# Kernel tuning notes

Hardware: AMD Instinct MI355X
Metric: run time of the kernel (lower is better)

Reference implementation:

```python
import jax, jax.numpy as jnp
import numpy as np

N_IN, N_LAT, LEN_T, N_SHIFT = 128, 21, 51, 50
N_HID, BATCH = 4, 2048


def identity_init(n_rows, n_cols):
    A = np.zeros((n_rows, n_cols), np.float32)
    if n_rows >= n_cols:
        k = n_rows - n_cols + 1
        for c in range(n_cols):
            A[c:c + k, c] = 1.0 / k
    else:
        k = n_cols - n_rows + 1
        for r in range(n_rows):
            A[r, r:r + k] = 1.0 / k
    return jnp.asarray(A)


def setup_inputs() -> dict:
    key = jax.random.key(0)
    ks = jax.random.split(key, 8)
    s = 0.05
    return {
        'inputs': jax.random.normal(ks[0], (BATCH, LEN_T, N_IN), dtype=jnp.float32),
        'enc_W': jax.random.normal(ks[1], (N_HID, N_IN, N_IN), dtype=jnp.float32) * s,
        'enc_b': jnp.zeros((N_HID, N_IN), jnp.float32),
        'enc_Wout': jax.random.normal(ks[2], (N_IN, N_IN), dtype=jnp.float32) * s,
        'enc_bout': jnp.zeros((N_IN,), jnp.float32),
        'dec_W': jax.random.normal(ks[3], (N_HID, N_IN, N_IN), dtype=jnp.float32) * s,
        'dec_b': jnp.zeros((N_HID, N_IN), jnp.float32),
        'dec_Wout': jax.random.normal(ks[4], (N_IN, N_IN), dtype=jnp.float32) * s,
        'dec_bout': jnp.zeros((N_IN,), jnp.float32),
        'W_enc_inner': identity_init(N_IN, N_LAT),
        'L': jnp.eye(N_LAT, dtype=jnp.float32),
        'W_dec_inner': identity_init(N_LAT, N_IN),
    }


def res_block(x, Ws, bs, Wout, bout):
    # DenseResBlock: ReLU hidden dense stack + linear output + identity skip
    h = x
    for i in range(Ws.shape[0]):
        h = jax.nn.relu(h @ Ws[i] + bs[i])
    return h @ Wout + bout + x


def reference(inputs, enc_W, enc_b, enc_Wout, enc_bout,
              dec_W, dec_b, dec_Wout, dec_bout,
              W_enc_inner, L, W_dec_inner):
    B = inputs.shape[0]
    len_pred = LEN_T - N_SHIFT  # = 1

    # ---- autoencoder branch (all timesteps flattened into rows) ----
    auto_in = inputs.reshape(-1, N_IN)                       # [B*T, n_in]
    part_enc = res_block(auto_in, enc_W, enc_b, enc_Wout, enc_bout)
    full_enc = part_enc @ W_enc_inner                        # [B*T, n_lat]
    part_dec = full_enc @ W_dec_inner                        # [B*T, n_in]
    autoencoder_output = res_block(part_dec, dec_W, dec_b, dec_Wout, dec_bout)
    autoencoder_output = autoencoder_output.reshape(B, LEN_T, N_IN)
    outer_auto_output = res_block(part_enc, dec_W, dec_b, dec_Wout, dec_bout)
    outer_auto_output = outer_auto_output.reshape(B, LEN_T, N_IN)

    # ---- prediction branch: recurrent application of Koopman operator L ----
    pred_in = inputs[:, :len_pred, :].reshape(-1, N_IN)      # [B*len_pred, n_in]
    cur = res_block(pred_in, enc_W, enc_b, enc_Wout, enc_bout) @ W_enc_inner

    def step(cur_enc, _):
        adv = cur_enc @ L                                    # [B*len_pred, n_lat]
        dec = res_block(adv @ W_dec_inner, dec_W, dec_b, dec_Wout, dec_bout)
        return adv, dec

    _, preds = jax.lax.scan(step, cur, None, length=N_SHIFT)  # [S, B*lp, n_in]
    preds = preds.reshape(N_SHIFT, B, len_pred, N_IN)
    predictions = preds.transpose(1, 0, 2, 3).reshape(B, N_SHIFT * len_pred, N_IN)

    return autoencoder_output, outer_auto_output, predictions
```

## Files before the change

### kernel.cpp

```cpp
#include <hip/hip_runtime.h>
#include <stdint.h>


typedef _Float16 h8 __attribute__((ext_vector_type(8)));
typedef _Float16 h4 __attribute__((ext_vector_type(4)));
typedef float    f4 __attribute__((ext_vector_type(4)));

#define ROWS_AUTO 104448
#define NT64      1632

#define WT_ENCW      0
#define WT_ENCWOUT   (4*16384)
#define WT_DECW      (5*16384)
#define WT_DECWOUT   (9*16384)
#define WT_COMB      (10*16384)

#define MFULL_OFF_B 0x60000
#define ACH_OFF_B   0x200000
#define PE_OFF_B    0x220000
#define PD_OFF_B    0x1C00000

#define H0 0
#define H1 16384
#define H2 32768
#define LDSE 51712
#define HP 0
#define P0 16384
#define P1 32768
#define P2 49152
#define LDSP 68096

#define hsw(rl, c) ((rl)*256 + ((((c)) ^ ((rl) & 7)) << 4))

#define PIN(B) asm volatile("" : "+v"(B[0]), "+v"(B[1]), "+v"(B[2]), "+v"(B[3]), \
                                 "+v"(B[4]), "+v"(B[5]), "+v"(B[6]), "+v"(B[7]))

__device__ __forceinline__ f4 mfma16(h8 a, h8 b, f4 c) {
  return __builtin_amdgcn_mfma_f32_16x16x32_f16(a, b, c, 0, 0, 0);
}
__device__ __forceinline__ h8 cvt8(f4 a, f4 b) {
  h8 r;
  r[0]=(_Float16)a[0]; r[1]=(_Float16)a[1]; r[2]=(_Float16)a[2]; r[3]=(_Float16)a[3];
  r[4]=(_Float16)b[0]; r[5]=(_Float16)b[1]; r[6]=(_Float16)b[2]; r[7]=(_Float16)b[3];
  return r;
}
__device__ __forceinline__ void loadW(h8 B[8], const _Float16* gW, int nbase, int r15, int hi) {
#pragma unroll
  for (int nt = 0; nt < 2; ++nt)
#pragma unroll
    for (int ks = 0; ks < 4; ++ks)
      B[nt*4+ks] = *(const h8*)(gW + (size_t)(nbase + nt*16 + r15)*128 + ks*32 + hi*8);
}

__device__ __forceinline__ void mmF4s(const char* sm, int hb, const h8 B[8],
                                      f4 acc[4][2], int r15, int hi) {
#pragma unroll
  for (int rt = 0; rt < 4; ++rt) { acc[rt][0] = (f4){0,0,0,0}; acc[rt][1] = (f4){0,0,0,0}; }
#pragma unroll
  for (int ks = 0; ks < 4; ++ks) {
    int c = ks*4 + hi;
    h8 a[4];
#pragma unroll
    for (int rt = 0; rt < 4; ++rt) a[rt] = *(const h8*)(sm + hb + hsw(rt*16 + r15, c));
#pragma unroll
    for (int rt = 0; rt < 4; ++rt) {
      acc[rt][0] = mfma16(B[ks],   a[rt], acc[rt][0]);
      acc[rt][1] = mfma16(B[4+ks], a[rt], acc[rt][1]);
    }
  }
}

__device__ __forceinline__ void hw4s(char* sm, int hb, int wbase, const f4 acc[4][2],
                                     const float* bl, int bo, int r15, int hi) {
  f4 bb0 = *(const f4*)(bl + bo + wbase + hi*4);
  f4 bb1 = *(const f4*)(bl + bo + wbase + 16 + hi*4);
  int bo2 = (hi & 1) * 8;
#pragma unroll
  for (int nt = 0; nt < 2; ++nt) {
    int c = ((wbase + nt*16) >> 3) + (hi >> 1);
    f4 bb = nt ? bb1 : bb0;
#pragma unroll
    for (int rt = 0; rt < 4; ++rt) {
      int row = rt*16 + r15;
      h4 p;
#pragma unroll
      for (int d = 0; d < 4; ++d) p[d] = (_Float16)fmaxf(acc[rt][nt][d] + bb[d], 0.f);
      *(h4*)(sm + hb + row*256 + ((c ^ (row & 7)) << 4) + bo2) = p;
    }
  }
}
__device__ __forceinline__ void hw4r(char* sm, int hb, int wbase, const f4 acc[4][2],
                                     int r15, int hi) {
  int bo2 = (hi & 1) * 8;
#pragma unroll
  for (int nt = 0; nt < 2; ++nt) {
    int c = ((wbase + nt*16) >> 3) + (hi >> 1);
#pragma unroll
    for (int rt = 0; rt < 4; ++rt) {
      int row = rt*16 + r15;
      h4 p;
#pragma unroll
      for (int d = 0; d < 4; ++d) p[d] = (_Float16)acc[rt][nt][d];
      *(h4*)(sm + hb + row*256 + ((c ^ (row & 7)) << 4) + bo2) = p;
    }
  }
}


__global__ __launch_bounds__(512) void k_prep(
    const float* __restrict__ encW, const float* __restrict__ encWout,
    const float* __restrict__ decW, const float* __restrict__ decWout,
    const float* __restrict__ L,
    _Float16* __restrict__ wt, float* __restrict__ ach) {
  __shared__ float chA[441], chB[441];
  int m = blockIdx.y, tid = threadIdx.x;
  if (m == 10) {
    if (blockIdx.x != 0) return;
    if (tid < 441) chA[tid] = L[tid];
    __syncthreads();
    for (int s = 0; s < 50; ++s) {
      if (tid < 441) ach[s*441 + tid] = chA[tid];
      if (s == 49) break;
      if (tid < 441) {
        int i = tid / 21, j = tid % 21; float a = 0.f;
        for (int k = 0; k < 21; ++k) a += chA[i*21 + k] * L[k*21 + j];
        chB[tid] = a;
      }
      __syncthreads();
      if (tid < 441) chA[tid] = chB[tid];
      __syncthreads();
    }
    return;
  }
  int idx = blockIdx.x*512 + tid;
  if (idx >= 16384) return;
  const float* src; _Float16* dst;
  if (m < 4)       { src = encW + m*16384;     dst = wt + WT_ENCW + m*16384; }
  else if (m == 4) { src = encWout;            dst = wt + WT_ENCWOUT; }
  else if (m < 9)  { src = decW + (m-5)*16384; dst = wt + WT_DECW + (m-5)*16384; }
  else             { src = decWout;            dst = wt + WT_DECWOUT; }
  int n = idx >> 7, k = idx & 127;
  dst[idx] = (_Float16)src[k*128 + n];
}

__global__ __launch_bounds__(512) void k_aux(
    const float* __restrict__ ach, const float* __restrict__ wencI,
    const float* __restrict__ wdecI,
    _Float16* __restrict__ mfull, _Float16* __restrict__ wt) {
  __shared__ float T1[2688];
  __shared__ float sa[441];
  int s = blockIdx.x, t = threadIdx.x;
  if (s < 50) {
    if (t < 441) sa[t] = ach[s*441 + t];
    __syncthreads();
    for (int idx = t; idx < 2688; idx += 512) {
      int k = idx / 21, j = idx % 21;
      float a = 0.f;
      for (int u = 0; u < 21; ++u) a += wencI[k*21 + u] * sa[u*21 + j];
      T1[idx] = a;
    }
  } else {
    for (int idx = t; idx < 2688; idx += 512) T1[idx] = wencI[idx];
  }
  __syncthreads();
  _Float16* dst = (s < 50) ? (mfull + (size_t)s*16384) : (wt + WT_COMB);
  for (int idx = t; idx < 16384; idx += 512) {
    int n = idx >> 7, k = idx & 127;
    float a = 0.f;
    for (int j = 0; j < 21; ++j) a += T1[k*21 + j] * wdecI[j*128 + n];
    dst[idx] = (_Float16)a;
  }
}


__global__ __launch_bounds__(256, 2) void k_enc(
    const float* __restrict__ x, const _Float16* __restrict__ wt,
    const float* __restrict__ enc_b, const float* __restrict__ enc_bout,
    _Float16* __restrict__ pe_ws, _Float16* __restrict__ pd_ws) {
  __shared__ char sm[LDSE];
  float* bl = (float*)(sm + 49152);
  int tid = threadIdx.x, lane = tid & 63;
  int r15 = lane & 15, hi = lane >> 4;
  int wbase = (tid >> 6) * 32;
  h8 B0[8], B1[8], B2[8], B3[8], B4[8], B5[8];
  loadW(B0, wt + WT_ENCW,           wbase, r15, hi);
  loadW(B1, wt + WT_ENCW + 16384,   wbase, r15, hi);
  loadW(B2, wt + WT_ENCW + 2*16384, wbase, r15, hi);
  loadW(B3, wt + WT_ENCW + 3*16384, wbase, r15, hi);
  loadW(B4, wt + WT_ENCWOUT,        wbase, r15, hi);
  loadW(B5, wt + WT_COMB,           wbase, r15, hi);
  PIN(B0); PIN(B1); PIN(B2); PIN(B3); PIN(B4); PIN(B5);
  bl[tid] = enc_b[tid]; bl[256 + tid] = enc_b[256 + tid];
  if (tid < 128) bl[512 + tid] = enc_bout[tid];
  f4 acc[4][2];

  for (int t = blockIdx.x; t < NT64; t += gridDim.x) {
    size_t rb = (size_t)t * 64;
#pragma unroll
    for (int i = 0; i < 4; ++i) {
      int idx = i*256 + tid, rl = idx >> 4, c = idx & 15;
      const float* s = x + (rb + rl)*128 + c*8;
      f4 v0 = *(const f4*)s, v1 = *(const f4*)(s + 4);
      *(h8*)(sm + H0 + hsw(rl, c)) = cvt8(v0, v1);
    }
    __syncthreads();
    mmF4s(sm, H0, B0, acc, r15, hi); hw4s(sm, H1, wbase, acc, bl, 0,   r15, hi); __syncthreads();
    mmF4s(sm, H1, B1, acc, r15, hi); hw4s(sm, H2, wbase, acc, bl, 128, r15, hi); __syncthreads();
    mmF4s(sm, H2, B2, acc, r15, hi); hw4s(sm, H1, wbase, acc, bl, 256, r15, hi); __syncthreads();
    mmF4s(sm, H1, B3, acc, r15, hi); hw4s(sm, H2, wbase, acc, bl, 384, r15, hi); __syncthreads();
    mmF4s(sm, H2, B4, acc, r15, hi);
    {
      f4 bb0 = *(const f4*)(bl + 512 + wbase + hi*4);
      f4 bb1 = *(const f4*)(bl + 512 + wbase + 16 + hi*4);
      int bo2 = (hi & 1) * 8;
#pragma unroll
      for (int nt = 0; nt < 2; ++nt) {
        int c = ((wbase + nt*16) >> 3) + (hi >> 1);
        f4 bb = nt ? bb1 : bb0;
#pragma unroll
        for (int rt = 0; rt < 4; ++rt) {
          int row = rt*16 + r15;
          int soff = row*256 + ((c ^ (row & 7)) << 4) + bo2;
          h4 sk = *(const h4*)(sm + H0 + soff);
          h4 p;
#pragma unroll
          for (int d = 0; d < 4; ++d) p[d] = (_Float16)(acc[rt][nt][d] + bb[d] + (float)sk[d]);
          *(h4*)(sm + H1 + soff) = p;
        }
      }
    }
    __syncthreads();
    {
      char* g = (char*)(pe_ws) + (size_t)t*16384;
#pragma unroll
      for (int i = 0; i < 4; ++i) { int off = (i*256 + tid)*16;
        *(f4*)(g + off) = *(const f4*)(sm + H1 + off); }
    }
    mmF4s(sm, H1, B5, acc, r15, hi);
    hw4r(sm, H2, wbase, acc, r15, hi);
    __syncthreads();
    {
      char* g = (char*)(pd_ws) + (size_t)t*16384;
#pragma unroll
      for (int i = 0; i < 4; ++i) { int off = (i*256 + tid)*16;
        *(f4*)(g + off) = *(const f4*)(sm + H2 + off); }
    }
  }
}


__global__ __launch_bounds__(256, 2) void k_dec(
    const _Float16* __restrict__ wt, const _Float16* __restrict__ pe_ws,
    const _Float16* __restrict__ pd_ws,
    const float* __restrict__ dec_b, const float* __restrict__ dec_bout,
    float* __restrict__ out1, float* __restrict__ out2) {
  __shared__ char sm[LDSE];
  float* bl = (float*)(sm + 49152);
  int tid = threadIdx.x, lane = tid & 63;
  int r15 = lane & 15, hi = lane >> 4;
  int wbase = (tid >> 6) * 32;
  h8 B0[8], B1[8], B2[8], B3[8], B4[8];
  loadW(B0, wt + WT_DECW,           wbase, r15, hi);
  loadW(B1, wt + WT_DECW + 16384,   wbase, r15, hi);
  loadW(B2, wt + WT_DECW + 2*16384, wbase, r15, hi);
  loadW(B3, wt + WT_DECW + 3*16384, wbase, r15, hi);
  loadW(B4, wt + WT_DECWOUT,        wbase, r15, hi);
  PIN(B0); PIN(B1); PIN(B2); PIN(B3); PIN(B4);
  bl[tid] = dec_b[tid]; bl[256 + tid] = dec_b[256 + tid];
  if (tid < 128) bl[512 + tid] = dec_bout[tid];
  f4 acc[4][2];

  for (int u = blockIdx.x; u < 2*NT64; u += gridDim.x) {
    int t = (u >= NT64) ? u - NT64 : u;
    const char* src = (const char*)((u >= NT64) ? pd_ws : pe_ws) + (size_t)t*16384;
    float* dst = ((u >= NT64) ? out1 : out2) + (size_t)t*64*128;
#pragma unroll
    for (int i = 0; i < 4; ++i) {
      int off = (i*256 + tid)*16;
      *(f4*)(sm + H0 + off) = *(const f4*)(src + off);
    }
    __syncthreads();
    mmF4s(sm, H0, B0, acc, r15, hi); hw4s(sm, H1, wbase, acc, bl, 0,   r15, hi); __syncthreads();
    mmF4s(sm, H1, B1, acc, r15, hi); hw4s(sm, H2, wbase, acc, bl, 128, r15, hi); __syncthreads();
    mmF4s(sm, H2, B2, acc, r15, hi); hw4s(sm, H1, wbase, acc, bl, 256, r15, hi); __syncthreads();
    mmF4s(sm, H1, B3, acc, r15, hi); hw4s(sm, H2, wbase, acc, bl, 384, r15, hi); __syncthreads();
    mmF4s(sm, H2, B4, acc, r15, hi);
    __syncthreads();
    {
      f4 bb0 = *(const f4*)(bl + 512 + wbase + hi*4);
      f4 bb1 = *(const f4*)(bl + 512 + wbase + 16 + hi*4);
      int bo2 = (hi & 1) * 8;
#pragma unroll
      for (int nt = 0; nt < 2; ++nt) {
        int c = ((wbase + nt*16) >> 3) + (hi >> 1);
        int q = (wbase >> 2) + nt*4 + hi;
        f4 bb = nt ? bb1 : bb0;
#pragma unroll
        for (int rt = 0; rt < 4; ++rt) {
          int row = rt*16 + r15;
          h4 sk = *(const h4*)(sm + H0 + row*256 + ((c ^ (row & 7)) << 4) + bo2);
          f4 v;
#pragma unroll
          for (int d = 0; d < 4; ++d) v[d] = acc[rt][nt][d] + bb[d] + (float)sk[d];
          *(f4*)(sm + H1 + row*512 + ((q ^ ((row & 7) << 2)) << 4)) = v;
        }
      }
    }
    __syncthreads();
    {
#pragma unroll
      for (int i = 0; i < 8; ++i) {
        int idx = i*256 + tid, row = idx >> 5, q = idx & 31;
        f4 v = *(const f4*)(sm + H1 + row*512 + ((q ^ ((row & 7) << 2)) << 4));
        *(f4*)(dst + (size_t)row*128 + q*4) = v;
      }
    }
  }
}


__global__ __launch_bounds__(256, 2) void k_pred(
    const _Float16* __restrict__ pe_ws, const _Float16* __restrict__ wt,
    const _Float16* __restrict__ mfull,
    const float* __restrict__ dec_b, const float* __restrict__ dec_bout,
    float* __restrict__ out3) {
  __shared__ char sm[LDSP];
  float* bl = (float*)(sm + 65536);
  int tid = threadIdx.x, lane = tid & 63;
  int r15 = lane & 15, hi = lane >> 4;
  int wbase = (tid >> 6) * 32;
  h8 B0[8], B1[8], B2[8], B3[8], B4[8];
  loadW(B0, wt + WT_DECW,           wbase, r15, hi);
  loadW(B1, wt + WT_DECW + 16384,   wbase, r15, hi);
  loadW(B2, wt + WT_DECW + 2*16384, wbase, r15, hi);
  loadW(B3, wt + WT_DECW + 3*16384, wbase, r15, hi);
  loadW(B4, wt + WT_DECWOUT,        wbase, r15, hi);
  PIN(B0); PIN(B1); PIN(B2); PIN(B3); PIN(B4);
  bl[tid] = dec_b[tid]; bl[256 + tid] = dec_b[256 + tid];
  if (tid < 128) bl[512 + tid] = dec_bout[tid];
  f4 acc[4][2];

  int rtile = blockIdx.x / 10, chunk = blockIdx.x % 10;
#pragma unroll
  for (int i = 0; i < 4; ++i) {
    int idx = i*256 + tid, rl = idx >> 4, c = idx & 15;
    int rg = rtile*64 + rl;
    int r  = rg * 51;
    const char* sp = (const char*)pe_ws + (size_t)(r >> 6)*16384
                   + (r & 63)*256 + ((c ^ ((r & 63) & 7)) << 4);
    *(f4*)(sm + HP + hsw(rl, c)) = *(const f4*)sp;
  }
  __syncthreads();

  for (int s = chunk*5; s < chunk*5 + 5; ++s) {
    h8 Bm[8];
    loadW(Bm, mfull + (size_t)s*16384, wbase, r15, hi);
    mmF4s(sm, HP, Bm, acc, r15, hi);
    hw4r(sm, P0, wbase, acc, r15, hi);
    __syncthreads();
    mmF4s(sm, P0, B0, acc, r15, hi); hw4s(sm, P1, wbase, acc, bl, 0,   r15, hi); __syncthreads();
    mmF4s(sm, P1, B1, acc, r15, hi); hw4s(sm, P2, wbase, acc, bl, 128, r15, hi); __syncthreads();
    mmF4s(sm, P2, B2, acc, r15, hi); hw4s(sm, P1, wbase, acc, bl, 256, r15, hi); __syncthreads();
    mmF4s(sm, P1, B3, acc, r15, hi); hw4s(sm, P2, wbase, acc, bl, 384, r15, hi); __syncthreads();
    mmF4s(sm, P2, B4, acc, r15, hi);
    __syncthreads();
    {
      f4 bb0 = *(const f4*)(bl + 512 + wbase + hi*4);
      f4 bb1 = *(const f4*)(bl + 512 + wbase + 16 + hi*4);
      int bo2 = (hi & 1) * 8;
#pragma unroll
      for (int nt = 0; nt < 2; ++nt) {
        int c = ((wbase + nt*16) >> 3) + (hi >> 1);
        int q = (wbase >> 2) + nt*4 + hi;
        f4 bb = nt ? bb1 : bb0;
#pragma unroll
        for (int rt = 0; rt < 4; ++rt) {
          int row = rt*16 + r15;
          h4 sk = *(const h4*)(sm + P0 + row*256 + ((c ^ (row & 7)) << 4) + bo2);
          f4 v;
#pragma unroll
          for (int d = 0; d < 4; ++d) v[d] = acc[rt][nt][d] + bb[d] + (float)sk[d];
          *(f4*)(sm + P1 + row*512 + ((q ^ ((row & 7) << 2)) << 4)) = v;
        }
      }
    }
    __syncthreads();
    {
#pragma unroll
      for (int i = 0; i < 8; ++i) {
        int idx = i*256 + tid, row = idx >> 5, q = idx & 31;
        size_t b = (size_t)(rtile*64 + row);
        f4 v = *(const f4*)(sm + P1 + row*512 + ((q ^ ((row & 7) << 2)) << 4));
        *(f4*)(out3 + (b*50 + s)*128 + q*4) = v;
      }
    }
    __syncthreads();
  }
}


extern "C" void kernel_launch(void* const* d_in, const int* in_sizes, int n_in,
                              void* d_out, int out_size, void* d_ws, size_t ws_size,
                              hipStream_t stream) {
  const float* x        = (const float*)d_in[0];
  const float* encW     = (const float*)d_in[1];
  const float* enc_b    = (const float*)d_in[2];
  const float* encWout  = (const float*)d_in[3];
  const float* enc_bout = (const float*)d_in[4];
  const float* decW     = (const float*)d_in[5];
  const float* dec_b    = (const float*)d_in[6];
  const float* decWout  = (const float*)d_in[7];
  const float* dec_bout = (const float*)d_in[8];
  const float* wencI    = (const float*)d_in[9];
  const float* L        = (const float*)d_in[10];
  const float* wdecI    = (const float*)d_in[11];

  char* ws = (char*)d_ws;
  _Float16* wt    = (_Float16*)ws;
  _Float16* mfull = (_Float16*)(ws + MFULL_OFF_B);
  float*    ach   = (float*)(ws + ACH_OFF_B);
  _Float16* pe_ws = (_Float16*)(ws + PE_OFF_B);
  _Float16* pd_ws = (_Float16*)(ws + PD_OFF_B);

  float* out1 = (float*)d_out;
  float* out2 = out1 + (size_t)ROWS_AUTO*128;
  float* out3 = out2 + (size_t)ROWS_AUTO*128;

  hipLaunchKernelGGL(k_prep, dim3(32, 11), dim3(512), 0, stream,
                     encW, encWout, decW, decWout, L, wt, ach);
  hipLaunchKernelGGL(k_aux, dim3(51), dim3(512), 0, stream,
                     ach, wencI, wdecI, mfull, wt);
  hipLaunchKernelGGL(k_enc, dim3(512), dim3(256), 0, stream,
                     x, wt, enc_b, enc_bout, pe_ws, pd_ws);
  hipLaunchKernelGGL(k_pred, dim3(320), dim3(256), 0, stream,
                     pe_ws, wt, mfull, dec_b, dec_bout, out3);
  hipLaunchKernelGGL(k_dec, dim3(512), dim3(256), 0, stream,
                     wt, pe_ws, pd_ws, dec_b, dec_bout, out1, out2);
}
```

Baseline: 232.9 us.

## Fuse decoder and prediction kernels, recompute part_dec in-block instead of via workspace

```diff
diff --git a/kernel.cpp b/kernel.cpp
--- a/kernel.cpp
+++ b/kernel.cpp
@@ -8,6 +8,7 @@
 
 #define ROWS_AUTO 104448
 #define NT64      1632
+#define NUNITS    1952
 
 #define WT_ENCW      0
 #define WT_ENCWOUT   (4*16384)
@@ -18,17 +19,14 @@
 #define MFULL_OFF_B 0x60000
 #define ACH_OFF_B   0x200000
 #define PE_OFF_B    0x220000
-#define PD_OFF_B    0x1C00000
+#define PET0_OFF_B  0x1C00000
 
 #define H0 0
 #define H1 16384
 #define H2 32768
+#define H3 49152
 #define LDSE 51712
-#define HP 0
-#define P0 16384
-#define P1 32768
-#define P2 49152
-#define LDSP 68096
+#define LDSD 68096
 
 #define hsw(rl, c) ((rl)*256 + ((((c)) ^ ((rl) & 7)) << 4))
 
@@ -105,6 +103,43 @@
     }
   }
 }
+
+__device__ __forceinline__ void epi_store(char* sm, int hskip, int htr, int wbase,
+                                          const f4 acc[4][2], const float* bl,
+                                          float* dst, int rstride,
+                                          int tid, int r15, int hi) {
+  f4 bb0 = *(const f4*)(bl + 512 + wbase + hi*4);
+  f4 bb1 = *(const f4*)(bl + 512 + wbase + 16 + hi*4);
+  int bo2 = (hi & 1) * 8;
+#pragma unroll
+  for (int nt = 0; nt < 2; ++nt) {
+    int c = ((wbase + nt*16) >> 3) + (hi >> 1);
+    int q = (wbase >> 2) + nt*4 + hi;
+    f4 bb = nt ? bb1 : bb0;
+#pragma unroll
+    for (int rt = 0; rt < 4; ++rt) {
+      int row = rt*16 + r15;
+      h4 sk = *(const h4*)(sm + hskip + row*256 + ((c ^ (row & 7)) << 4) + bo2);
+      f4 v;
+#pragma unroll
+      for (int d = 0; d < 4; ++d) v[d] = acc[rt][nt][d] + bb[d] + (float)sk[d];
+      *(f4*)(sm + htr + row*512 + ((q ^ ((row & 7) << 2)) << 4)) = v;
+    }
+  }
+  __syncthreads();
+#pragma unroll
+  for (int i = 0; i < 8; ++i) {
+    int idx = i*256 + tid, row = idx >> 5, q = idx & 31;
+    f4 v = *(const f4*)(sm + htr + row*512 + ((q ^ ((row & 7) << 2)) << 4));
+    *(f4*)(dst + (size_t)row*rstride + q*4) = v;
+  }
+}
+
+#define LAYD(HIN, HOUT, BW, BO) do {                                 \
+    mmF4s(sm, HIN, BW, acc, r15, hi);                                \
+    hw4s(sm, HOUT, wbase, acc, bl, BO, r15, hi);                     \
+    __syncthreads();                                                 \
+  } while (0)
 
 
 __global__ __launch_bounds__(512) void k_prep(
@@ -176,116 +211,36 @@
 __global__ __launch_bounds__(256, 2) void k_enc(
     const float* __restrict__ x, const _Float16* __restrict__ wt,
     const float* __restrict__ enc_b, const float* __restrict__ enc_bout,
-    _Float16* __restrict__ pe_ws, _Float16* __restrict__ pd_ws) {
-  __shared__ char sm[LDSE];
-  float* bl = (float*)(sm + 49152);
-  int tid = threadIdx.x, lane = tid & 63;
-  int r15 = lane & 15, hi = lane >> 4;
-  int wbase = (tid >> 6) * 32;
-  h8 B0[8], B1[8], B2[8], B3[8], B4[8], B5[8];
-  loadW(B0, wt + WT_ENCW,           wbase, r15, hi);
-  loadW(B1, wt + WT_ENCW + 16384,   wbase, r15, hi);
-  loadW(B2, wt + WT_ENCW + 2*16384, wbase, r15, hi);
-  loadW(B3, wt + WT_ENCW + 3*16384, wbase, r15, hi);
-  loadW(B4, wt + WT_ENCWOUT,        wbase, r15, hi);
-  loadW(B5, wt + WT_COMB,           wbase, r15, hi);
-  PIN(B0); PIN(B1); PIN(B2); PIN(B3); PIN(B4); PIN(B5);
-  bl[tid] = enc_b[tid]; bl[256 + tid] = enc_b[256 + tid];
-  if (tid < 128) bl[512 + tid] = enc_bout[tid];
-  f4 acc[4][2];
-
-  for (int t = blockIdx.x; t < NT64; t += gridDim.x) {
-    size_t rb = (size_t)t * 64;
-#pragma unroll
-    for (int i = 0; i < 4; ++i) {
-      int idx = i*256 + tid, rl = idx >> 4, c = idx & 15;
-      const float* s = x + (rb + rl)*128 + c*8;
-      f4 v0 = *(const f4*)s, v1 = *(const f4*)(s + 4);
-      *(h8*)(sm + H0 + hsw(rl, c)) = cvt8(v0, v1);
-    }
-    __syncthreads();
-    mmF4s(sm, H0, B0, acc, r15, hi); hw4s(sm, H1, wbase, acc, bl, 0,   r15, hi); __syncthreads();
-    mmF4s(sm, H1, B1, acc, r15, hi); hw4s(sm, H2, wbase, acc, bl, 128, r15, hi); __syncthreads();
-    mmF4s(sm, H2, B2, acc, r15, hi); hw4s(sm, H1, wbase, acc, bl, 256, r15, hi); __syncthreads();
-    mmF4s(sm, H1, B3, acc, r15, hi); hw4s(sm, H2, wbase, acc, bl, 384, r15, hi); __syncthreads();
-    mmF4s(sm, H2, B4, acc, r15, hi);
-    {
-      f4 bb0 = *(const f4*)(bl + 512 + wbase + hi*4);
-      f4 bb1 = *(const f4*)(bl + 512 + wbase + 16 + hi*4);
-      int bo2 = (hi & 1) * 8;
-#pragma unroll
-      for (int nt = 0; nt < 2; ++nt) {
-        int c = ((wbase + nt*16) >> 3) + (hi >> 1);
-        f4 bb = nt ? bb1 : bb0;
-#pragma unroll
-        for (int rt = 0; rt < 4; ++rt) {
-          int row = rt*16 + r15;
-          int soff = row*256 + ((c ^ (row & 7)) << 4) + bo2;
-          h4 sk = *(const h4*)(sm + H0 + soff);
-          h4 p;
-#pragma unroll
-          for (int d = 0; d < 4; ++d) p[d] = (_Float16)(acc[rt][nt][d] + bb[d] + (float)sk[d]);
-          *(h4*)(sm + H1 + soff) = p;
-        }
-      }
-    }
-    __syncthreads();
-    {
-      char* g = (char*)(pe_ws) + (size_t)t*16384;
-#pragma unroll
-      for (int i = 0; i < 4; ++i) { int off = (i*256 + tid)*16;
-        *(f4*)(g + off) = *(const f4*)(sm + H1 + off); }
-    }
-    mmF4s(sm, H1, B5, acc, r15, hi);
-    hw4r(sm, H2, wbase, acc, r15, hi);
-    __syncthreads();
-    {
-      char* g = (char*)(pd_ws) + (size_t)t*16384;
-#pragma unroll
-      for (int i = 0; i < 4; ++i) { int off = (i*256 + tid)*16;
-        *(f4*)(g + off) = *(const f4*)(sm + H2 + off); }
-    }
-  }
-}
-
-
-__global__ __launch_bounds__(256, 2) void k_dec(
-    const _Float16* __restrict__ wt, const _Float16* __restrict__ pe_ws,
-    const _Float16* __restrict__ pd_ws,
-    const float* __restrict__ dec_b, const float* __restrict__ dec_bout,
-    float* __restrict__ out1, float* __restrict__ out2) {
+    _Float16* __restrict__ pe_ws, _Float16* __restrict__ pet0) {
   __shared__ char sm[LDSE];
   float* bl = (float*)(sm + 49152);
   int tid = threadIdx.x, lane = tid & 63;
   int r15 = lane & 15, hi = lane >> 4;
   int wbase = (tid >> 6) * 32;
   h8 B0[8], B1[8], B2[8], B3[8], B4[8];
-  loadW(B0, wt + WT_DECW,           wbase, r15, hi);
-  loadW(B1, wt + WT_DECW + 16384,   wbase, r15, hi);
-  loadW(B2, wt + WT_DECW + 2*16384, wbase, r15, hi);
-  loadW(B3, wt + WT_DECW + 3*16384, wbase, r15, hi);
-  loadW(B4, wt + WT_DECWOUT,        wbase, r15, hi);
+  loadW(B0, wt + WT_ENCW,           wbase, r15, hi);
+  loadW(B1, wt + WT_ENCW + 16384,   wbase, r15, hi);
+  loadW(B2, wt + WT_ENCW + 2*16384, wbase, r15, hi);
+  loadW(B3, wt + WT_ENCW + 3*16384, wbase, r15, hi);
+  loadW(B4, wt + WT_ENCWOUT,        wbase, r15, hi);
   PIN(B0); PIN(B1); PIN(B2); PIN(B3); PIN(B4);
-  bl[tid] = dec_b[tid]; bl[256 + tid] = dec_b[256 + tid];
-  if (tid < 128) bl[512 + tid] = dec_bout[tid];
+  bl[tid] = enc_b[tid]; bl[256 + tid] = enc_b[256 + tid];
+  if (tid < 128) bl[512 + tid] = enc_bout[tid];
   f4 acc[4][2];
 
-  for (int u = blockIdx.x; u < 2*NT64; u += gridDim.x) {
-    int t = (u >= NT64) ? u - NT64 : u;
-    const char* src = (const char*)((u >= NT64) ? pd_ws : pe_ws) + (size_t)t*16384;
-    float* dst = ((u >= NT64) ? out1 : out2) + (size_t)t*64*128;
+  for (int t = blockIdx.x; t < NT64; t += gridDim.x) {
+    size_t rb = (size_t)t * 64;
 #pragma unroll
     for (int i = 0; i < 4; ++i) {
-      int off = (i*256 + tid)*16;
-      *(f4*)(sm + H0 + off) = *(const f4*)(src + off);
-    }
-    __syncthreads();
-    mmF4s(sm, H0, B0, acc, r15, hi); hw4s(sm, H1, wbase, acc, bl, 0,   r15, hi); __syncthreads();
-    mmF4s(sm, H1, B1, acc, r15, hi); hw4s(sm, H2, wbase, acc, bl, 128, r15, hi); __syncthreads();
-    mmF4s(sm, H2, B2, acc, r15, hi); hw4s(sm, H1, wbase, acc, bl, 256, r15, hi); __syncthreads();
-    mmF4s(sm, H1, B3, acc, r15, hi); hw4s(sm, H2, wbase, acc, bl, 384, r15, hi); __syncthreads();
+      int idx = i*256 + tid, rl = idx >> 4, c = idx & 15;
+      const float* s = x + (rb + rl)*128 + c*8;
+      f4 v0 = *(const f4*)s, v1 = *(const f4*)(s + 4);
+      *(h8*)(sm + H0 + hsw(rl, c)) = cvt8(v0, v1);
+    }
+    __syncthreads();
+    LAYD(H0, H1, B0, 0); LAYD(H1, H2, B1, 128);
+    LAYD(H2, H1, B2, 256); LAYD(H1, H2, B3, 384);
     mmF4s(sm, H2, B4, acc, r15, hi);
-    __syncthreads();
     {
       f4 bb0 = *(const f4*)(bl + 512 + wbase + hi*4);
       f4 bb1 = *(const f4*)(bl + 512 + wbase + 16 + hi*4);
@@ -293,38 +248,45 @@
 #pragma unroll
       for (int nt = 0; nt < 2; ++nt) {
         int c = ((wbase + nt*16) >> 3) + (hi >> 1);
-        int q = (wbase >> 2) + nt*4 + hi;
         f4 bb = nt ? bb1 : bb0;
 #pragma unroll
         for (int rt = 0; rt < 4; ++rt) {
           int row = rt*16 + r15;
-          h4 sk = *(const h4*)(sm + H0 + row*256 + ((c ^ (row & 7)) << 4) + bo2);
-          f4 v;
-#pragma unroll
-          for (int d = 0; d < 4; ++d) v[d] = acc[rt][nt][d] + bb[d] + (float)sk[d];
-          *(f4*)(sm + H1 + row*512 + ((q ^ ((row & 7) << 2)) << 4)) = v;
+          int soff = row*256 + ((c ^ (row & 7)) << 4) + bo2;
+          h4 sk = *(const h4*)(sm + H0 + soff);
+          h4 p;
+#pragma unroll
+          for (int d = 0; d < 4; ++d) p[d] = (_Float16)(acc[rt][nt][d] + bb[d] + (float)sk[d]);
+          *(h4*)(sm + H1 + soff) = p;
         }
       }
     }
     __syncthreads();
     {
-#pragma unroll
-      for (int i = 0; i < 8; ++i) {
-        int idx = i*256 + tid, row = idx >> 5, q = idx & 31;
-        f4 v = *(const f4*)(sm + H1 + row*512 + ((q ^ ((row & 7) << 2)) << 4));
-        *(f4*)(dst + (size_t)row*128 + q*4) = v;
-      }
-    }
-  }
-}
-
-
-__global__ __launch_bounds__(256, 2) void k_pred(
-    const _Float16* __restrict__ pe_ws, const _Float16* __restrict__ wt,
-    const _Float16* __restrict__ mfull,
+      char* g = (char*)(pe_ws) + (size_t)t*16384;
+#pragma unroll
+      for (int i = 0; i < 4; ++i) {
+        int idx = i*256 + tid, off = idx*16;
+        f4 v = *(const f4*)(sm + H1 + off);
+        *(f4*)(g + off) = v;
+        int rl = idx >> 4, slot = idx & 15;
+        size_t rg = rb + (size_t)rl;
+        if (rg % 51u == 0u) {
+          int c = slot ^ (rl & 7);
+          *(f4*)((char*)pet0 + (rg/51u)*256 + c*16) = v;
+        }
+      }
+    }
+  }
+}
+
+
+__global__ __launch_bounds__(256, 2) void k_decpred(
+    const _Float16* __restrict__ wt, const _Float16* __restrict__ pe_ws,
+    const _Float16* __restrict__ pet0, const _Float16* __restrict__ mfull,
     const float* __restrict__ dec_b, const float* __restrict__ dec_bout,
-    float* __restrict__ out3) {
-  __shared__ char sm[LDSP];
+    float* __restrict__ out1, float* __restrict__ out2, float* __restrict__ out3) {
+  __shared__ char sm[LDSD];
   float* bl = (float*)(sm + 65536);
   int tid = threadIdx.x, lane = tid & 63;
   int r15 = lane & 15, hi = lane >> 4;
@@ -340,61 +302,61 @@
   if (tid < 128) bl[512 + tid] = dec_bout[tid];
   f4 acc[4][2];
 
-  int rtile = blockIdx.x / 10, chunk = blockIdx.x % 10;
-#pragma unroll
-  for (int i = 0; i < 4; ++i) {
-    int idx = i*256 + tid, rl = idx >> 4, c = idx & 15;
-    int rg = rtile*64 + rl;
-    int r  = rg * 51;
-    const char* sp = (const char*)pe_ws + (size_t)(r >> 6)*16384
-                   + (r & 63)*256 + ((c ^ ((r & 63) & 7)) << 4);
-    *(f4*)(sm + HP + hsw(rl, c)) = *(const f4*)sp;
-  }
-  __syncthreads();
-
-  for (int s = chunk*5; s < chunk*5 + 5; ++s) {
-    h8 Bm[8];
-    loadW(Bm, mfull + (size_t)s*16384, wbase, r15, hi);
-    mmF4s(sm, HP, Bm, acc, r15, hi);
-    hw4r(sm, P0, wbase, acc, r15, hi);
-    __syncthreads();
-    mmF4s(sm, P0, B0, acc, r15, hi); hw4s(sm, P1, wbase, acc, bl, 0,   r15, hi); __syncthreads();
-    mmF4s(sm, P1, B1, acc, r15, hi); hw4s(sm, P2, wbase, acc, bl, 128, r15, hi); __syncthreads();
-    mmF4s(sm, P2, B2, acc, r15, hi); hw4s(sm, P1, wbase, acc, bl, 256, r15, hi); __syncthreads();
-    mmF4s(sm, P1, B3, acc, r15, hi); hw4s(sm, P2, wbase, acc, bl, 384, r15, hi); __syncthreads();
-    mmF4s(sm, P2, B4, acc, r15, hi);
-    __syncthreads();
-    {
-      f4 bb0 = *(const f4*)(bl + 512 + wbase + hi*4);
-      f4 bb1 = *(const f4*)(bl + 512 + wbase + 16 + hi*4);
-      int bo2 = (hi & 1) * 8;
-#pragma unroll
-      for (int nt = 0; nt < 2; ++nt) {
-        int c = ((wbase + nt*16) >> 3) + (hi >> 1);
-        int q = (wbase >> 2) + nt*4 + hi;
-        f4 bb = nt ? bb1 : bb0;
-#pragma unroll
-        for (int rt = 0; rt < 4; ++rt) {
-          int row = rt*16 + r15;
-          h4 sk = *(const h4*)(sm + P0 + row*256 + ((c ^ (row & 7)) << 4) + bo2);
-          f4 v;
-#pragma unroll
-          for (int d = 0; d < 4; ++d) v[d] = acc[rt][nt][d] + bb[d] + (float)sk[d];
-          *(f4*)(sm + P1 + row*512 + ((q ^ ((row & 7) << 2)) << 4)) = v;
+  for (int u = blockIdx.x; u < NUNITS; u += gridDim.x) {
+    __syncthreads();
+    if (u < NT64) {
+      const char* src = (const char*)pe_ws + (size_t)u*16384;
+      float* d2 = out2 + (size_t)u*64*128;
+      float* d1 = out1 + (size_t)u*64*128;
+#pragma unroll
+      for (int i = 0; i < 4; ++i) {
+        int off = (i*256 + tid)*16;
+        *(f4*)(sm + H0 + off) = *(const f4*)(src + off);
+      }
+      __syncthreads();
+      LAYD(H0, H1, B0, 0); LAYD(H1, H2, B1, 128);
+      LAYD(H2, H1, B2, 256); LAYD(H1, H2, B3, 384);
+      mmF4s(sm, H2, B4, acc, r15, hi);
+      __syncthreads();
+      epi_store(sm, H0, H1, wbase, acc, bl, d2, 128, tid, r15, hi);
+      {
+        h8 Bc[8];
+        loadW(Bc, wt + WT_COMB, wbase, r15, hi);
+        mmF4s(sm, H0, Bc, acc, r15, hi);
+      }
+      hw4r(sm, H3, wbase, acc, r15, hi);
+      __syncthreads();
+      LAYD(H3, H0, B0, 0); LAYD(H0, H1, B1, 128);
+      LAYD(H1, H0, B2, 256); LAYD(H0, H1, B3, 384);
+      mmF4s(sm, H1, B4, acc, r15, hi);
+      __syncthreads();
+      epi_store(sm, H3, H0, wbase, acc, bl, d1, 128, tid, r15, hi);
+    } else {
+      int p = u - NT64, rtile = p / 10, chunk = p % 10;
+#pragma unroll
+      for (int i = 0; i < 4; ++i) {
+        int idx = i*256 + tid, rl = idx >> 4, c = idx & 15;
+        f4 v = *(const f4*)((const char*)pet0 + (size_t)(rtile*64 + rl)*256 + c*16);
+        *(f4*)(sm + H0 + hsw(rl, c)) = v;
+      }
+      __syncthreads();
+      for (int s = chunk*5; s < chunk*5 + 5; ++s) {
+        {
+          h8 Bm[8];
+          loadW(Bm, mfull + (size_t)s*16384, wbase, r15, hi);
+          mmF4s(sm, H0, Bm, acc, r15, hi);
         }
-      }
-    }
-    __syncthreads();
-    {
-#pragma unroll
-      for (int i = 0; i < 8; ++i) {
-        int idx = i*256 + tid, row = idx >> 5, q = idx & 31;
-        size_t b = (size_t)(rtile*64 + row);
-        f4 v = *(const f4*)(sm + P1 + row*512 + ((q ^ ((row & 7) << 2)) << 4));
-        *(f4*)(out3 + (b*50 + s)*128 + q*4) = v;
-      }
-    }
-    __syncthreads();
+        hw4r(sm, H1, wbase, acc, r15, hi);
+        __syncthreads();
+        LAYD(H1, H2, B0, 0); LAYD(H2, H3, B1, 128);
+        LAYD(H3, H2, B2, 256); LAYD(H2, H3, B3, 384);
+        mmF4s(sm, H3, B4, acc, r15, hi);
+        __syncthreads();
+        epi_store(sm, H1, H2, wbase, acc, bl,
+                  out3 + ((size_t)rtile*64*50 + s)*128, 50*128, tid, r15, hi);
+        __syncthreads();
+      }
+    }
   }
 }
 
@@ -420,7 +382,7 @@
   _Float16* mfull = (_Float16*)(ws + MFULL_OFF_B);
   float*    ach   = (float*)(ws + ACH_OFF_B);
   _Float16* pe_ws = (_Float16*)(ws + PE_OFF_B);
-  _Float16* pd_ws = (_Float16*)(ws + PD_OFF_B);
+  _Float16* pet0  = (_Float16*)(ws + PET0_OFF_B);
 
   float* out1 = (float*)d_out;
   float* out2 = out1 + (size_t)ROWS_AUTO*128;
@@ -431,9 +393,7 @@
   hipLaunchKernelGGL(k_aux, dim3(51), dim3(512), 0, stream,
                      ach, wencI, wdecI, mfull, wt);
   hipLaunchKernelGGL(k_enc, dim3(512), dim3(256), 0, stream,
-                     x, wt, enc_b, enc_bout, pe_ws, pd_ws);
-  hipLaunchKernelGGL(k_pred, dim3(320), dim3(256), 0, stream,
-                     pe_ws, wt, mfull, dec_b, dec_bout, out3);
-  hipLaunchKernelGGL(k_dec, dim3(512), dim3(256), 0, stream,
-                     wt, pe_ws, pd_ws, dec_b, dec_bout, out1, out2);
-}
+                     x, wt, enc_b, enc_bout, pe_ws, pet0);
+  hipLaunchKernelGGL(k_decpred, dim3(512), dim3(256), 0, stream,
+                     wt, pe_ws, pet0, mfull, dec_b, dec_bout, out1, out2, out3);
+}
```

New measurement: 224.6 us. -3.6%, faster.
